# Optimization experiments

Measured on AMD Instinct MI355X. Metric: run time of the kernel, lower is better.

The kernel has to match this reference:

```python
import jax, jax.numpy as jnp
import numpy as np

T, D, H, Z = 16384, 100, 50, 64
LN_EPS = 1e-6


def _ln(x, s, b):
    m = x.mean(-1, keepdims=True)
    v = ((x - m) ** 2).mean(-1, keepdims=True)
    return (x - m) / jnp.sqrt(v + LN_EPS) * s + b


def _gru_ln_scan(y, Wi, Wh, ls, lb):
    # Precompute all input projections once: [T, 3H]
    xi = y @ Wi
    h0 = jnp.zeros((Wh.shape[0],), y.dtype)

    def step(h, xi_t):
        hh = h @ Wh
        xr, xz, xn = jnp.split(xi_t, 3)
        hr, hz, hn = jnp.split(hh, 3)
        r = jax.nn.sigmoid(_ln(xr, ls[0], lb[0]) + _ln(hr, ls[1], lb[1]))
        z = jax.nn.sigmoid(_ln(xz, ls[2], lb[2]) + _ln(hz, ls[3], lb[3]))
        n = jnp.tanh(_ln(xn, ls[4], lb[4]) + r * _ln(hn, ls[5], lb[5]))
        h_new = (1.0 - z) * n + z * h
        return h_new, h_new

    _, hs = jax.lax.scan(step, h0, xi)
    return hs  # [T, H]


def setup_inputs() -> dict:
    key = jax.random.key(0)
    ks = jax.random.split(key, 6)
    sI = 1.0 / jnp.sqrt(jnp.float32(D))
    sH = 1.0 / jnp.sqrt(jnp.float32(H))
    sD = 1.0 / jnp.sqrt(jnp.float32(2 * H))
    return {
        "y": jax.random.normal(ks[0], (T, D), jnp.float32),
        "Wi_f": jax.random.normal(ks[1], (D, 3 * H), jnp.float32) * sI,
        "Wh_f": jax.random.normal(ks[2], (H, 3 * H), jnp.float32) * sH,
        "ln_s_f": jnp.ones((6, H), jnp.float32),
        "ln_b_f": jnp.zeros((6, H), jnp.float32),
        "Wi_b": jax.random.normal(ks[3], (D, 3 * H), jnp.float32) * sI,
        "Wh_b": jax.random.normal(ks[4], (H, 3 * H), jnp.float32) * sH,
        "ln_s_b": jnp.ones((6, H), jnp.float32),
        "ln_b_b": jnp.zeros((6, H), jnp.float32),
        "Wd": jax.random.normal(ks[5], (2 * H, 2 * Z), jnp.float32) * sD,
        "bd": jnp.zeros((2 * Z,), jnp.float32),
    }


def reference(y, Wi_f, Wh_f, ln_s_f, ln_b_f, Wi_b, Wh_b, ln_s_b, ln_b_b, Wd, bd):
    fwd = _gru_ln_scan(y, Wi_f, Wh_f, ln_s_f, ln_b_f)                       # [T, H]
    bwd = jnp.flip(_gru_ln_scan(jnp.flip(y, 0), Wi_b, Wh_b, ln_s_b, ln_b_b), 0)
    cc = jnp.concatenate([fwd, bwd], axis=-1)                               # [T, 2H]
    out = cc @ Wd + bd                                                      # [T, 2Z]
    z = Wd.shape[1] // 2
    mu, vflat = out[:, :z], out[:, z:]
    ev = jnp.exp(vflat)
    eye = jnp.eye(z, dtype=y.dtype)
    Sigma = eye * (ev + 1e-6)[:, None, :]   # diag(exp(v)+1e-6) per timestep
    J = eye * (1.0 / ev)[:, None, :]        # diag(1/exp(v)) per timestep
    h = mu / ev                             # J @ mu for diagonal J
    return Sigma, mu, J, h
```

## Files before the change

kernel.cpp:

```cpp
#include <hip/hip_runtime.h>

#define TT 16384
#define DD 100
#define HH 50
#define XG_STRIDE 160

#define CL 16
#define NCHUNK (TT / CL)
#define BURN 64

#define XROWS 16

#define WS_XG 0
#define WS_HS (2 * TT * XG_STRIDE)

#define OFF_MU ((size_t)TT * 64 * 64)
#define OFF_J  (OFF_MU + (size_t)TT * 64)
#define OFF_H  (OFF_J + (size_t)TT * 64 * 64)

typedef float v2f __attribute__((ext_vector_type(2)));

template <int CTRL>
__device__ __forceinline__ float dpp_add(float x) {
    const int y = __builtin_amdgcn_update_dpp(
        0, __builtin_bit_cast(int, x), CTRL, 0xf, 0xf, false);
    return x + __builtin_bit_cast(float, y);
}
__device__ __forceinline__ float wave_sum63(float x) {
    x = dpp_add<0x111>(x);
    x = dpp_add<0x112>(x);
    x = dpp_add<0x114>(x);
    x = dpp_add<0x118>(x);
    x = dpp_add<0x142>(x);
    x = dpp_add<0x143>(x);
    return x;
}
__device__ __forceinline__ float bcast_lane(float x, int l) {
    return __builtin_bit_cast(float,
        __builtin_amdgcn_readlane(__builtin_bit_cast(int, x), l));
}
__device__ __forceinline__ float fold_mean(float w, int L, int lane) {
    const float s = wave_sum63(w);
    const float cm = bcast_lane(s, 63) * 0.02f;
    return (lane == L) ? cm : w;
}

__global__ __launch_bounds__(192) void xprep_kernel(
    const float* __restrict__ y,
    const float* __restrict__ Wi_f, const float* __restrict__ Wi_b,
    const float* __restrict__ ls_f, const float* __restrict__ lb_f,
    const float* __restrict__ ls_b, const float* __restrict__ lb_b,
    float* __restrict__ xg)
{
    const int t0  = blockIdx.x * XROWS;
    const int dir = blockIdx.y;
    const float* __restrict__ Wi = dir ? Wi_b : Wi_f;
    const float* __restrict__ ls = dir ? ls_b : ls_f;
    const float* __restrict__ lb = dir ? lb_b : lb_f;

    __shared__ __align__(16) float yst[DD][XROWS];
    const int tid = threadIdx.x;

    for (int idx = tid; idx < DD * XROWS; idx += 192) {
        const int r = idx / DD;
        const int k = idx - r * DD;
        const int row = dir ? (TT - 1 - (t0 + r)) : (t0 + r);
        yst[k][r] = y[(size_t)row * DD + k];
    }
    __syncthreads();

    const int g    = tid >> 6;
    const int lane = tid & 63;
    const bool act = lane < HH;
    const int col  = g * 50 + (act ? lane : 0);

    float acc[XROWS];
    #pragma unroll
    for (int r = 0; r < XROWS; ++r) acc[r] = 0.f;

    #pragma unroll 2
    for (int k = 0; k < DD; ++k) {
        const float w = Wi[k * 150 + col];
        const float4* yr = (const float4*)&yst[k][0];
        const float4 A = yr[0], B = yr[1], C = yr[2], D = yr[3];
        acc[0]  = fmaf(w, A.x, acc[0]);  acc[1]  = fmaf(w, A.y, acc[1]);
        acc[2]  = fmaf(w, A.z, acc[2]);  acc[3]  = fmaf(w, A.w, acc[3]);
        acc[4]  = fmaf(w, B.x, acc[4]);  acc[5]  = fmaf(w, B.y, acc[5]);
        acc[6]  = fmaf(w, B.z, acc[6]);  acc[7]  = fmaf(w, B.w, acc[7]);
        acc[8]  = fmaf(w, C.x, acc[8]);  acc[9]  = fmaf(w, C.y, acc[9]);
        acc[10] = fmaf(w, C.z, acc[10]); acc[11] = fmaf(w, C.w, acc[11]);
        acc[12] = fmaf(w, D.x, acc[12]); acc[13] = fmaf(w, D.y, acc[13]);
        acc[14] = fmaf(w, D.z, acc[14]); acc[15] = fmaf(w, D.w, acc[15]);
    }

    const int lrow = g * 100 + (act ? lane : 0);
    const float sc = ls[lrow], bi = lb[lrow];
    #pragma unroll
    for (int r = 0; r < XROWS; ++r) {
        const float a  = act ? acc[r] : 0.f;
        const float s  = bcast_lane(wave_sum63(a), 63);
        const float s2 = bcast_lane(wave_sum63(a * a), 63);
        const float mean = s * 0.02f;
        const float var  = s2 * 0.02f - mean * mean;
        const float rstd = rsqrtf(var + 1e-6f);
        if (act)
            xg[((size_t)dir * TT + (t0 + r)) * XG_STRIDE + col] =
                (acc[r] - mean) * rstd * sc + bi;
    }
}

__global__ __launch_bounds__(64, 1) void scan_kernel(
    const float* __restrict__ xg,
    const float* __restrict__ Wh_f, const float* __restrict__ Wh_b,
    const float* __restrict__ ls_f, const float* __restrict__ lb_f,
    const float* __restrict__ ls_b, const float* __restrict__ lb_b,
    float* __restrict__ hs)
{
    const int dir = blockIdx.y;
    const float* __restrict__ Wh = dir ? Wh_b : Wh_f;
    const float* __restrict__ ls = dir ? ls_b : ls_f;
    const float* __restrict__ lb = dir ? lb_b : lb_f;
    const float* __restrict__ xgd = xg + (size_t)dir * TT * XG_STRIDE;
    float* __restrict__ hsd = hs + (size_t)dir * TT * 64;

    const int lane = threadIdx.x;
    const bool act = lane < HH;

    const int cstart = blockIdx.x * CL;
    const int t0 = (cstart >= BURN) ? (cstart - BURN) : 0;
    const int tend = cstart + CL;

    __shared__ __align__(16) float hb[52];
    if (lane < 52) hb[lane] = 0.f;

    v2f wr2[26], wz2[26], wn2[26];
    #pragma unroll
    for (int p = 0; p < 26; ++p) {
        wr2[p] = (v2f){0.f, 0.f};
        wz2[p] = (v2f){0.f, 0.f};
        wn2[p] = (v2f){0.f, 0.f};
    }
    float s1 = 0.f, b1 = 0.f, s3 = 0.f, b3 = 0.f, s5 = 0.f, b5 = 0.f;
    if (act) {
        #pragma unroll
        for (int k = 0; k < HH; ++k) {
            const float a = Wh[k * 150 + lane];
            const float b = Wh[k * 150 + 50 + lane];
            const float c = Wh[k * 150 + 100 + lane];
            if (k & 1) { wr2[k >> 1].y = a; wz2[k >> 1].y = b; wn2[k >> 1].y = c; }
            else       { wr2[k >> 1].x = a; wz2[k >> 1].x = b; wn2[k >> 1].x = c; }
        }
        s1 = ls[50 + lane];  b1 = lb[50 + lane];
        s3 = ls[150 + lane]; b3 = lb[150 + lane];
        s5 = ls[250 + lane]; b5 = lb[250 + lane];
    }
    #pragma unroll
    for (int p = 0; p < 26; ++p) {
        wr2[p].x = fold_mean(wr2[p].x, 50, lane);
        wr2[p].y = fold_mean(wr2[p].y, 50, lane);
        wz2[p].x = fold_mean(wz2[p].x, 51, lane);
        wz2[p].y = fold_mean(wz2[p].y, 51, lane);
        wn2[p].x = fold_mean(wn2[p].x, 52, lane);
        wn2[p].y = fold_mean(wn2[p].y, 52, lane);
    }

    float hreg = 0.f;
    const int xl = act ? lane : 0;
    const float* __restrict__ x0 = xgd + (size_t)t0 * XG_STRIDE;
    float xr = x0[xl], xz = x0[50 + xl], xn = x0[100 + xl];
    float pxr = x0[XG_STRIDE + xl];
    float pxz = x0[XG_STRIDE + 50 + xl];
    float pxn = x0[XG_STRIDE + 100 + xl];

    #pragma unroll 1
    for (int t = t0; t < tend; ++t) {
        const int tp = (t + 2 < TT) ? (t + 2) : (TT - 1);
        const float* __restrict__ xp = xgd + (size_t)tp * XG_STRIDE;
        const float qxr = xp[xl], qxz = xp[50 + xl], qxn = xp[100 + xl];

        v2f ar0 = {0.f, 0.f}, ar1 = {0.f, 0.f};
        v2f az0 = {0.f, 0.f}, az1 = {0.f, 0.f};
        v2f an0 = {0.f, 0.f}, an1 = {0.f, 0.f};
        const float4* hb4 = reinterpret_cast<const float4*>(hb);
        #pragma unroll
        for (int q = 0; q < 13; ++q) {
            const float4 hv = hb4[q];
            const v2f h0 = {hv.x, hv.y};
            const v2f h1 = {hv.z, hv.w};
            ar0 = __builtin_elementwise_fma(h0, wr2[2 * q],     ar0);
            ar1 = __builtin_elementwise_fma(h1, wr2[2 * q + 1], ar1);
            az0 = __builtin_elementwise_fma(h0, wz2[2 * q],     az0);
            az1 = __builtin_elementwise_fma(h1, wz2[2 * q + 1], az1);
            an0 = __builtin_elementwise_fma(h0, wn2[2 * q],     an0);
            an1 = __builtin_elementwise_fma(h1, wn2[2 * q + 1], an1);
        }
        const float ar = (ar0.x + ar0.y) + (ar1.x + ar1.y);
        const float az = (az0.x + az0.y) + (az1.x + az1.y);
        const float an = (an0.x + an0.y) + (an1.x + an1.y);

        const float mr = bcast_lane(ar, 50);
        const float mz = bcast_lane(az, 51);
        const float mn = bcast_lane(an, 52);

        const float qrv = act ? ar * ar : 0.f;
        const float qzv = act ? az * az : 0.f;
        const float qnv = act ? an * an : 0.f;
        const float Sr = bcast_lane(wave_sum63(qrv), 63);
        const float Sz = bcast_lane(wave_sum63(qzv), 63);
        const float Sn = bcast_lane(wave_sum63(qnv), 63);

        const float i50 = 0.02f;
        const float vr = fmaf(-mr, mr, Sr * i50);
        const float vz = fmaf(-mz, mz, Sz * i50);
        const float vn = fmaf(-mn, mn, Sn * i50);
        const float rr = rsqrtf(vr + 1e-6f);
        const float rz = rsqrtf(vz + 1e-6f);
        const float rn = rsqrtf(vn + 1e-6f);
        const float hrl = (ar - mr) * rr * s1 + b1;
        const float hzl = (az - mz) * rz * s3 + b3;
        const float hnl = (an - mn) * rn * s5 + b5;

        const float r = __builtin_amdgcn_rcpf(1.f + __expf(-(xr + hrl)));
        const float z = __builtin_amdgcn_rcpf(1.f + __expf(-(xz + hzl)));
        const float e2 = __expf(2.f * (xn + r * hnl));
        const float n = 1.f - 2.f * __builtin_amdgcn_rcpf(e2 + 1.f);
        const float hnew = fmaf(z, hreg - n, n);

        if (act) {
            hb[lane] = hnew;
            if (t >= cstart) hsd[(size_t)t * 64 + lane] = hnew;
        }
        hreg = act ? hnew : 0.f;

        xr = pxr; xz = pxz; xn = pxn;
        pxr = qxr; pxz = qxz; pxn = qxn;
    }
}

__global__ __launch_bounds__(256) void outfill_kernel(
    const float* __restrict__ hs, const float* __restrict__ Wd,
    const float* __restrict__ bd, float* __restrict__ out)
{
    const int t = blockIdx.x;
    const int j = threadIdx.x;
    __shared__ float cc[DD];
    __shared__ float os[128];
    __shared__ float svv[64], jvv[64];
    if (j < 50)
        cc[j] = hs[(size_t)t * 64 + j];
    else if (j < 100)
        cc[j] = hs[(size_t)(TT + (TT - 1 - t)) * 64 + (j - 50)];
    __syncthreads();

    if (j < 128) {
        float acc = bd[j];
        #pragma unroll 4
        for (int k = 0; k < DD; ++k) acc = fmaf(cc[k], Wd[k * 128 + j], acc);
        os[j] = acc;
    }
    __syncthreads();

    if (j < 64) {
        const float mu  = os[j];
        const float evv = __expf(os[64 + j]);
        out[OFF_MU + (size_t)t * 64 + j] = mu;
        out[OFF_H  + (size_t)t * 64 + j] = mu / evv;
        svv[j] = evv + 1e-6f;
        jvv[j] = 1.f / evv;
    }
    __syncthreads();

    float4* __restrict__ so4 = (float4*)(out + (size_t)t * 4096);
    float4* __restrict__ jo4 = (float4*)(out + OFF_J + (size_t)t * 4096);
    #pragma unroll
    for (int q = j; q < 1024; q += 256) {
        const int i  = q >> 4;
        const int c  = (q & 15) << 2;
        const int d  = i - c;
        float4 s  = {0.f, 0.f, 0.f, 0.f};
        float4 jv = {0.f, 0.f, 0.f, 0.f};
        if (d >= 0 && d < 4) {
            const float se = svv[i], je = jvv[i];
            s.x  = (d == 0) ? se : 0.f;  s.y  = (d == 1) ? se : 0.f;
            s.z  = (d == 2) ? se : 0.f;  s.w  = (d == 3) ? se : 0.f;
            jv.x = (d == 0) ? je : 0.f;  jv.y = (d == 1) ? je : 0.f;
            jv.z = (d == 2) ? je : 0.f;  jv.w = (d == 3) ? je : 0.f;
        }
        so4[q] = s;
        jo4[q] = jv;
    }
}

extern "C" void kernel_launch(void* const* d_in, const int* in_sizes, int n_in,
                              void* d_out, int out_size, void* d_ws, size_t ws_size,
                              hipStream_t stream)
{
    const float* y    = (const float*)d_in[0];
    const float* Wi_f = (const float*)d_in[1];
    const float* Wh_f = (const float*)d_in[2];
    const float* ls_f = (const float*)d_in[3];
    const float* lb_f = (const float*)d_in[4];
    const float* Wi_b = (const float*)d_in[5];
    const float* Wh_b = (const float*)d_in[6];
    const float* ls_b = (const float*)d_in[7];
    const float* lb_b = (const float*)d_in[8];
    const float* Wd   = (const float*)d_in[9];
    const float* bd   = (const float*)d_in[10];

    float* out = (float*)d_out;
    float* ws  = (float*)d_ws;
    float* xg  = ws + WS_XG;
    float* hsb = ws + WS_HS;

    xprep_kernel<<<dim3(TT / XROWS, 2), dim3(192), 0, stream>>>(
        y, Wi_f, Wi_b, ls_f, lb_f, ls_b, lb_b, xg);
    scan_kernel<<<dim3(NCHUNK, 2), dim3(64), 0, stream>>>(
        xg, Wh_f, Wh_b, ls_f, lb_f, ls_b, lb_b, hsb);
    outfill_kernel<<<dim3(TT), dim3(256), 0, stream>>>(
        hsb, Wd, bd, out);
}
```

Baseline: 238.3 us.

## Overlap zero-fill of Sigma/J with xprep and scan, write only diagonals at the end

The bulk zero-fill of the two large T×64×64 diagonal matrices moves out of the final kernel. Extra blocks appended to the xprep and scan launches now do it, so the fill overlaps with the latency-bound scan. The output kernel then handles 8 timesteps per block, reusing each Wd load across 8 rows, and writes only the diagonal float4 entries. The risk is that the extra fill blocks compete with the scan blocks for bandwidth and compute units, and the results depend on ordering within the stream.

```diff
diff --git a/kernel.cpp b/kernel.cpp
--- a/kernel.cpp
+++ b/kernel.cpp
@@ -10,6 +10,7 @@
 #define BURN 64
 
 #define XROWS 16
+#define OROWS 8
 
 #define WS_XG 0
 #define WS_HS (2 * TT * XG_STRIDE)
@@ -50,16 +51,27 @@
     const float* __restrict__ Wi_f, const float* __restrict__ Wi_b,
     const float* __restrict__ ls_f, const float* __restrict__ lb_f,
     const float* __restrict__ ls_b, const float* __restrict__ lb_b,
-    float* __restrict__ xg)
+    float* __restrict__ xg, float* __restrict__ out)
 {
+    const int tid = threadIdx.x;
+    const int dir = blockIdx.y;
+
+    if (dir == 2) {
+        float4* __restrict__ so4 = (float4*)out;
+        const long QN = (long)TT * 1024;
+        const float4 zz = {0.f, 0.f, 0.f, 0.f};
+        const long stride = (long)gridDim.x * 192;
+        for (long q = (long)blockIdx.x * 192 + tid; q < QN; q += stride)
+            so4[q] = zz;
+        return;
+    }
+
     const int t0  = blockIdx.x * XROWS;
-    const int dir = blockIdx.y;
     const float* __restrict__ Wi = dir ? Wi_b : Wi_f;
     const float* __restrict__ ls = dir ? ls_b : ls_f;
     const float* __restrict__ lb = dir ? lb_b : lb_f;
 
     __shared__ __align__(16) float yst[DD][XROWS];
-    const int tid = threadIdx.x;
 
     for (int idx = tid; idx < DD * XROWS; idx += 192) {
         const int r = idx / DD;
@@ -114,8 +126,23 @@
     const float* __restrict__ Wh_f, const float* __restrict__ Wh_b,
     const float* __restrict__ ls_f, const float* __restrict__ lb_f,
     const float* __restrict__ ls_b, const float* __restrict__ lb_b,
-    float* __restrict__ hs)
+    float* __restrict__ hs, float* __restrict__ out)
 {
+    const int lane = threadIdx.x;
+
+    if (blockIdx.x >= NCHUNK) {
+        float4* __restrict__ jo4 = (float4*)(out + OFF_J);
+        const long QN = (long)TT * 1024;
+        const float4 zz = {0.f, 0.f, 0.f, 0.f};
+        const long nfb = (long)(gridDim.x - NCHUNK) * 2;
+        const long fb  = (long)blockIdx.y * (gridDim.x - NCHUNK)
+                       + (blockIdx.x - NCHUNK);
+        const long stride = nfb * 64;
+        for (long q = fb * 64 + lane; q < QN; q += stride)
+            jo4[q] = zz;
+        return;
+    }
+
     const int dir = blockIdx.y;
     const float* __restrict__ Wh = dir ? Wh_b : Wh_f;
     const float* __restrict__ ls = dir ? ls_b : ls_f;
@@ -123,7 +150,6 @@
     const float* __restrict__ xgd = xg + (size_t)dir * TT * XG_STRIDE;
     float* __restrict__ hsd = hs + (size_t)dir * TT * 64;
 
-    const int lane = threadIdx.x;
     const bool act = lane < HH;
 
     const int cstart = blockIdx.x * CL;
@@ -237,57 +263,74 @@
     }
 }
 
-__global__ __launch_bounds__(256) void outfill_kernel(
+__global__ __launch_bounds__(128) void outdiag_kernel(
     const float* __restrict__ hs, const float* __restrict__ Wd,
     const float* __restrict__ bd, float* __restrict__ out)
 {
-    const int t = blockIdx.x;
-    const int j = threadIdx.x;
-    __shared__ float cc[DD];
-    __shared__ float os[128];
-    __shared__ float svv[64], jvv[64];
-    if (j < 50)
-        cc[j] = hs[(size_t)t * 64 + j];
-    else if (j < 100)
-        cc[j] = hs[(size_t)(TT + (TT - 1 - t)) * 64 + (j - 50)];
+    const int t0 = blockIdx.x * OROWS;
+    const int j  = threadIdx.x;
+
+    __shared__ __align__(16) float ccs[DD][OROWS];
+    __shared__ float os[OROWS][128];
+
+    for (int idx = j; idx < DD * OROWS; idx += 128) {
+        const int k = idx >> 3;
+        const int r = idx & 7;
+        const int t = t0 + r;
+        ccs[k][r] = (k < 50)
+            ? hs[(size_t)t * 64 + k]
+            : hs[(size_t)(TT + (TT - 1 - t)) * 64 + (k - 50)];
+    }
     __syncthreads();
 
-    if (j < 128) {
-        float acc = bd[j];
-        #pragma unroll 4
-        for (int k = 0; k < DD; ++k) acc = fmaf(cc[k], Wd[k * 128 + j], acc);
-        os[j] = acc;
-    }
+    float acc[OROWS];
+    const float b = bd[j];
+    #pragma unroll
+    for (int r = 0; r < OROWS; ++r) acc[r] = b;
+
+    #pragma unroll 2
+    for (int k = 0; k < DD; ++k) {
+        const float w = Wd[k * 128 + j];
+        const float4* cr = (const float4*)&ccs[k][0];
+        const float4 A = cr[0], B4 = cr[1];
+        acc[0] = fmaf(w, A.x,  acc[0]); acc[1] = fmaf(w, A.y,  acc[1]);
+        acc[2] = fmaf(w, A.z,  acc[2]); acc[3] = fmaf(w, A.w,  acc[3]);
+        acc[4] = fmaf(w, B4.x, acc[4]); acc[5] = fmaf(w, B4.y, acc[5]);
+        acc[6] = fmaf(w, B4.z, acc[6]); acc[7] = fmaf(w, B4.w, acc[7]);
+    }
+    #pragma unroll
+    for (int r = 0; r < OROWS; ++r) os[r][j] = acc[r];
     __syncthreads();
 
     if (j < 64) {
-        const float mu  = os[j];
-        const float evv = __expf(os[64 + j]);
-        out[OFF_MU + (size_t)t * 64 + j] = mu;
-        out[OFF_H  + (size_t)t * 64 + j] = mu / evv;
-        svv[j] = evv + 1e-6f;
-        jvv[j] = 1.f / evv;
-    }
-    __syncthreads();
-
-    float4* __restrict__ so4 = (float4*)(out + (size_t)t * 4096);
-    float4* __restrict__ jo4 = (float4*)(out + OFF_J + (size_t)t * 4096);
-    #pragma unroll
-    for (int q = j; q < 1024; q += 256) {
-        const int i  = q >> 4;
-        const int c  = (q & 15) << 2;
-        const int d  = i - c;
-        float4 s  = {0.f, 0.f, 0.f, 0.f};
-        float4 jv = {0.f, 0.f, 0.f, 0.f};
-        if (d >= 0 && d < 4) {
-            const float se = svv[i], je = jvv[i];
-            s.x  = (d == 0) ? se : 0.f;  s.y  = (d == 1) ? se : 0.f;
-            s.z  = (d == 2) ? se : 0.f;  s.w  = (d == 3) ? se : 0.f;
-            jv.x = (d == 0) ? je : 0.f;  jv.y = (d == 1) ? je : 0.f;
-            jv.z = (d == 2) ? je : 0.f;  jv.w = (d == 3) ? je : 0.f;
-        }
-        so4[q] = s;
-        jo4[q] = jv;
+        const int d = j & 3;
+        #pragma unroll
+        for (int r = 0; r < OROWS; ++r) {
+            const int t = t0 + r;
+            const float mu  = os[r][j];
+            const float evv = __expf(os[r][64 + j]);
+            out[OFF_MU + (size_t)t * 64 + j] = mu;
+            out[OFF_H  + (size_t)t * 64 + j] = mu / evv;
+            const float se = evv + 1e-6f;
+            float4 s4;
+            s4.x = (d == 0) ? se : 0.f;  s4.y = (d == 1) ? se : 0.f;
+            s4.z = (d == 2) ? se : 0.f;  s4.w = (d == 3) ? se : 0.f;
+            ((float4*)out)[(size_t)t * 1024 + j * 16 + (j >> 2)] = s4;
+        }
+    } else {
+        const int i = j - 64;
+        const int d = i & 3;
+        float4* __restrict__ jo4 = (float4*)(out + OFF_J);
+        #pragma unroll
+        for (int r = 0; r < OROWS; ++r) {
+            const int t = t0 + r;
+            const float evv = __expf(os[r][j]);
+            const float je = 1.f / evv;
+            float4 j4;
+            j4.x = (d == 0) ? je : 0.f;  j4.y = (d == 1) ? je : 0.f;
+            j4.z = (d == 2) ? je : 0.f;  j4.w = (d == 3) ? je : 0.f;
+            jo4[(size_t)t * 1024 + i * 16 + (i >> 2)] = j4;
+        }
     }
 }
 
@@ -312,10 +355,10 @@
     float* xg  = ws + WS_XG;
     float* hsb = ws + WS_HS;
 
-    xprep_kernel<<<dim3(TT / XROWS, 2), dim3(192), 0, stream>>>(
-        y, Wi_f, Wi_b, ls_f, lb_f, ls_b, lb_b, xg);
-    scan_kernel<<<dim3(NCHUNK, 2), dim3(64), 0, stream>>>(
-        xg, Wh_f, Wh_b, ls_f, lb_f, ls_b, lb_b, hsb);
-    outfill_kernel<<<dim3(TT), dim3(256), 0, stream>>>(
+    xprep_kernel<<<dim3(TT / XROWS, 3), dim3(192), 0, stream>>>(
+        y, Wi_f, Wi_b, ls_f, lb_f, ls_b, lb_b, xg, out);
+    scan_kernel<<<dim3(NCHUNK + 1024, 2), dim3(64), 0, stream>>>(
+        xg, Wh_f, Wh_b, ls_f, lb_f, ls_b, lb_b, hsb, out);
+    outdiag_kernel<<<dim3(TT / OROWS), dim3(128), 0, stream>>>(
         hsb, Wd, bd, out);
 }
```

Measured after the change: 305.6 us. 1.28x slower.
